# Performance work log

Hardware: AMD Instinct MI355X
Metric: run time of the kernel (lower is better)

The kernel has to match this reference:

```python
import jax, jax.numpy as jnp
import numpy as np

DIM = 1024
H = 16
HD = DIM // H  # 64
EPS = 1e-6
B, N = 1, 2048


def setup_inputs() -> dict:
    key = jax.random.key(0)
    k1, k2, k3 = jax.random.split(key, 3)
    x = jax.random.normal(k1, (B, N, DIM), dtype=jnp.float32)
    qkv_w = jax.random.normal(k2, (3 * DIM, DIM), dtype=jnp.float32) * 0.02
    proj_w = jax.random.normal(k3, (DIM, DIM), dtype=jnp.float32) * 0.02
    alpha_log = jnp.zeros((H,), dtype=jnp.float32)  # torch init: zeros
    beta_log = jnp.zeros((H,), dtype=jnp.float32)
    return {"x": x, "qkv_w": qkv_w, "proj_w": proj_w,
            "alpha_log": alpha_log, "beta_log": beta_log}


def reference(x, qkv_w, proj_w, alpha_log, beta_log):
    b, n, c = x.shape
    # fused qkv projection (nn.Linear: y = x @ W.T), split into per-head q,k,v
    qkv = (x @ qkv_w.T).reshape(b, n, 3, H, HD).transpose(2, 0, 3, 1, 4)
    q, k, v = qkv[0], qkv[1], qkv[2]  # each [b,h,n,d]
    # positive ReLU feature map
    phi_q = jax.nn.relu(q) + EPS
    phi_k = jax.nn.relu(k) + EPS
    # causal prefix-sum of outer products phi_k v^T -> running state S_n
    kv = jnp.einsum('bhnd,bhne->bhnde', phi_k, v)   # [b,h,n,d,d]
    S = jnp.cumsum(kv, axis=2)                       # prefix sums over n
    out = jnp.einsum('bhnd,bhnde->bhne', phi_q, S)   # [b,h,n,d]
    # SteLLA normalization: per-head alpha'*beta'*sqrt(d) * prefix length
    alpha_p = jax.nn.softplus(alpha_log) + 1e-6
    beta_p = jax.nn.softplus(beta_log) + 1e-6
    scale = (alpha_p * beta_p * jnp.sqrt(jnp.float32(HD))).reshape(1, H, 1, 1)
    pos = jnp.arange(1, n + 1, dtype=x.dtype).reshape(1, 1, n, 1)
    denom = jnp.maximum(scale * pos, EPS)
    out = out / denom
    out = out.transpose(0, 2, 1, 3).reshape(b, n, c)
    return out @ proj_w.T  # output projection (dropout=0 -> identity)
```

## Files before the change

kernel.cpp:

```cpp
#include <hip/hip_runtime.h>
#include <math.h>

#define DIM 1024
#define NH 16
#define HD 64
#define SEQ 2048
#define CHUNK 128
#define NCHUNK (SEQ / CHUNK)
#define QKV_COLS (3 * DIM)

typedef __attribute__((ext_vector_type(8))) short bf16x8;
typedef __attribute__((ext_vector_type(4))) float f32x4;

__device__ __forceinline__ unsigned short f2bf(float f) {
  unsigned int u = __float_as_uint(f);
  u += 0x7FFF + ((u >> 16) & 1);
  return (unsigned short)(u >> 16);
}
__device__ __forceinline__ float bf2f(unsigned short s) {
  return __uint_as_float(((unsigned int)s) << 16);
}
__device__ __forceinline__ int swzb(int byte, int row) {
  return byte ^ ((row & 7) << 4);
}

__global__ __launch_bounds__(256) void convert_all(const float* __restrict__ x,
                                                   const float* __restrict__ qw,
                                                   const float* __restrict__ pw,
                                                   unsigned short* __restrict__ xb,
                                                   unsigned short* __restrict__ qwb,
                                                   unsigned short* __restrict__ pwb) {
  const int b = blockIdx.x;
  const float* in; unsigned short* out; int i;
  if (b < 2048)      { in = x;  out = xb;  i = b * 256 + threadIdx.x; }
  else if (b < 5120) { in = qw; out = qwb; i = (b - 2048) * 256 + threadIdx.x; }
  else               { in = pw; out = pwb; i = (b - 5120) * 256 + threadIdx.x; }
  float4 v = reinterpret_cast<const float4*>(in)[i];
  ushort4 o;
  o.x = f2bf(v.x); o.y = f2bf(v.y); o.z = f2bf(v.z); o.w = f2bf(v.w);
  reinterpret_cast<ushort4*>(out)[i] = o;
}

template <int BM, int BN, typename OutT>
__global__ __launch_bounds__(256) void gemm3_bt(const unsigned short* __restrict__ A,
                                                const unsigned short* __restrict__ W,
                                                OutT* __restrict__ C,
                                                int M, int Nn, int K) {
  constexpr int BK = 32;
  constexpr int MFR = BM / 32;
  constexpr int NFR = BN / 32;
  constexpr int ACH = BM / 64;
  constexpr int BCH = BN / 64;
  __shared__ unsigned short As[3][BM * BK];
  __shared__ unsigned short Bs[3][BN * BK];
  const int tid  = threadIdx.x;
  const int lane = tid & 63;
  const int wv   = tid >> 6;
  const int row0 = blockIdx.y * BM;
  const int col0 = blockIdx.x * BN;
  const int ln15 = lane & 15;
  const int lhi  = lane >> 4;
  const int wr = (wv >> 1) * (BM / 2);
  const int wc = (wv & 1) * (BN / 2);

  f32x4 acc[MFR][NFR] = {};

  auto stage = [&](int buf, int t) {
    const int k0 = t * BK;
#pragma unroll
    for (int tt = 0; tt < ACH; ++tt) {
      const int chunk = wv * ACH + tt;
      const int lid = chunk * 64 + lane;
      const int r  = lid >> 2;
      const int ke = (lid & 3) << 3;
      __builtin_amdgcn_global_load_lds(
          (const __attribute__((address_space(1))) void*)&A[(size_t)(row0 + r) * K + k0 + ke],
          (__attribute__((address_space(3))) void*)&As[buf][chunk * 512], 16, 0, 0);
    }
#pragma unroll
    for (int tt = 0; tt < BCH; ++tt) {
      const int chunk = wv * BCH + tt;
      const int lid = chunk * 64 + lane;
      const int r  = lid >> 2;
      const int ke = (lid & 3) << 3;
      __builtin_amdgcn_global_load_lds(
          (const __attribute__((address_space(1))) void*)&W[(size_t)(col0 + r) * K + k0 + ke],
          (__attribute__((address_space(3))) void*)&Bs[buf][chunk * 512], 16, 0, 0);
    }
  };

  const int nt = K / BK;
  stage(0, 0);
  stage(1, 1);
  for (int t = 0; t < nt; ++t) {
    if (t < nt - 1) {
      constexpr int L = ACH + BCH;
      if constexpr (L == 4)      asm volatile("s_waitcnt vmcnt(4)" ::: "memory");
      else if constexpr (L == 3) asm volatile("s_waitcnt vmcnt(3)" ::: "memory");
      else                       asm volatile("s_waitcnt vmcnt(2)" ::: "memory");
    } else {
      asm volatile("s_waitcnt vmcnt(0)" ::: "memory");
    }
    __builtin_amdgcn_s_barrier();
    if (t + 2 < nt) stage((t + 2) % 3, t + 2);
    const int cur = t % 3;
    bf16x8 a[MFR], b[NFR];
#pragma unroll
    for (int m = 0; m < MFR; ++m)
      a[m] = *reinterpret_cast<const bf16x8*>(&As[cur][(wr + m * 16 + ln15) * BK + lhi * 8]);
#pragma unroll
    for (int n = 0; n < NFR; ++n)
      b[n] = *reinterpret_cast<const bf16x8*>(&Bs[cur][(wc + n * 16 + ln15) * BK + lhi * 8]);
#pragma unroll
    for (int m = 0; m < MFR; ++m)
#pragma unroll
      for (int n = 0; n < NFR; ++n)
        acc[m][n] = __builtin_amdgcn_mfma_f32_16x16x32_bf16(a[m], b[n], acc[m][n], 0, 0, 0);
  }

  const int crow = lhi * 4;
  const int ccol = ln15;
#pragma unroll
  for (int m = 0; m < MFR; ++m)
#pragma unroll
    for (int n = 0; n < NFR; ++n)
#pragma unroll
      for (int r = 0; r < 4; ++r) {
        const size_t idx = (size_t)(row0 + wr + m * 16 + crow + r) * Nn + col0 + wc + n * 16 + ccol;
        if constexpr (sizeof(OutT) == 2) C[idx] = (OutT)f2bf(acc[m][n][r]);
        else                             C[idx] = acc[m][n][r];
      }
}

__global__ __launch_bounds__(256) void ckv_mfma_kernel(const unsigned short* __restrict__ qkv,
                                                       float* __restrict__ ckv) {
  const int h = blockIdx.x / NCHUNK;
  const int c = blockIdx.x % NCHUNK;
  const int tid  = threadIdx.x;
  const int lane = tid & 63;
  const int w    = tid >> 6;
  const int ln15 = lane & 15;
  const int lhi  = lane >> 4;

  __shared__ unsigned short kst[HD * CHUNK];
  __shared__ unsigned short vt[HD * CHUNK];

  for (int i = tid; i < CHUNK * HD / 4; i += 256) {
    const int r = i >> 4;
    const int d4 = (i & 15) << 2;
    const size_t base = (size_t)(c * CHUNK + r) * QKV_COLS + h * HD + d4;
    ushort4 k4 = *reinterpret_cast<const ushort4*>(&qkv[base + DIM]);
    ushort4 v4 = *reinterpret_cast<const ushort4*>(&qkv[base + 2 * DIM]);
#pragma unroll
    for (int j = 0; j < 4; ++j) {
      const int d = d4 + j;
      *reinterpret_cast<unsigned short*>((char*)kst + swzb(d * 256 + r * 2, d)) =
          f2bf(fmaxf(bf2f((&k4.x)[j]), 0.f) + 1e-6f);
      *reinterpret_cast<unsigned short*>((char*)vt + swzb(d * 256 + r * 2, d)) = (&v4.x)[j];
    }
  }
  __syncthreads();

  f32x4 acc[4] = {};
#pragma unroll
  for (int ks = 0; ks < 4; ++ks) {
    const int dr = w * 16 + ln15;
    bf16x8 a = *reinterpret_cast<const bf16x8*>((char*)kst + swzb(dr * 256 + (ks * 32 + lhi * 8) * 2, dr));
#pragma unroll
    for (int et = 0; et < 4; ++et) {
      const int er = et * 16 + ln15;
      bf16x8 b = *reinterpret_cast<const bf16x8*>((char*)vt + swzb(er * 256 + (ks * 32 + lhi * 8) * 2, er));
      acc[et] = __builtin_amdgcn_mfma_f32_16x16x32_bf16(a, b, acc[et], 0, 0, 0);
    }
  }
  const size_t base = (size_t)(h * NCHUNK + c) * (HD * HD);
#pragma unroll
  for (int et = 0; et < 4; ++et)
#pragma unroll
    for (int r = 0; r < 4; ++r)
      ckv[base + (size_t)(w * 16 + lhi * 4 + r) * HD + et * 16 + ln15] = acc[et][r];
}

__global__ __launch_bounds__(256) void attn_mfma_kernel(const unsigned short* __restrict__ qkv,
                                                        const float* __restrict__ ckv,
                                                        const float* __restrict__ alpha_log,
                                                        const float* __restrict__ beta_log,
                                                        unsigned short* __restrict__ attn_out) {
  const int h = blockIdx.x / NCHUNK;
  const int c = blockIdx.x % NCHUNK;
  const int tid  = threadIdx.x;
  const int lane = tid & 63;
  const int w    = tid >> 6;
  const int ln15 = lane & 15;
  const int lhi  = lane >> 4;

  __shared__ unsigned short ks[CHUNK * HD];
  __shared__ unsigned short vst[HD * 256];
  __shared__ unsigned short ps[CHUNK * CHUNK];

  float sp[16];
#pragma unroll
  for (int p = 0; p < 16; ++p) sp[p] = 0.f;
  {
    const float* cb = ckv + (size_t)h * NCHUNK * (HD * HD) + tid * 16;
    for (int cc = 0; cc < c; ++cc) {
      const float4* p4 = reinterpret_cast<const float4*>(cb + (size_t)cc * (HD * HD));
#pragma unroll
      for (int q = 0; q < 4; ++q) {
        float4 t = p4[q];
        sp[q * 4 + 0] += t.x; sp[q * 4 + 1] += t.y;
        sp[q * 4 + 2] += t.z; sp[q * 4 + 3] += t.w;
      }
    }
  }
  {
    const int d = tid >> 2;
#pragma unroll
    for (int j = 0; j < 16; ++j) {
      const int e = (tid & 3) * 16 + j;
      const float sv = sp[j];
      const unsigned short hi = f2bf(sv);
      const unsigned short lo = f2bf(sv - bf2f(hi));
      *reinterpret_cast<unsigned short*>((char*)vst + swzb(e * 512 + d * 2, e)) = hi;
      *reinterpret_cast<unsigned short*>((char*)vst + swzb(e * 512 + (64 + d) * 2, e)) = lo;
    }
  }

  for (int i = tid; i < CHUNK * HD / 4; i += 256) {
    const int r = i >> 4;
    const int d4 = (i & 15) << 2;
    const size_t base = (size_t)(c * CHUNK + r) * QKV_COLS + h * HD + d4;
    ushort4 k4 = *reinterpret_cast<const ushort4*>(&qkv[base + DIM]);
    ushort4 v4 = *reinterpret_cast<const ushort4*>(&qkv[base + 2 * DIM]);
    ushort4 pk4;
    pk4.x = f2bf(fmaxf(bf2f(k4.x), 0.f) + 1e-6f);
    pk4.y = f2bf(fmaxf(bf2f(k4.y), 0.f) + 1e-6f);
    pk4.z = f2bf(fmaxf(bf2f(k4.z), 0.f) + 1e-6f);
    pk4.w = f2bf(fmaxf(bf2f(k4.w), 0.f) + 1e-6f);
    *reinterpret_cast<ushort4*>((char*)ks + swzb(r * 128 + d4 * 2, r)) = pk4;
#pragma unroll
    for (int j = 0; j < 4; ++j) {
      const int e = d4 + j;
      *reinterpret_cast<unsigned short*>((char*)vst + swzb(e * 512 + (128 + r) * 2, e)) = (&v4.x)[j];
    }
  }
  bf16x8 qf[2][2];
#pragma unroll
  for (int m = 0; m < 2; ++m)
#pragma unroll
    for (int kk = 0; kk < 2; ++kk) {
      const size_t gq = (size_t)(c * CHUNK + w * 32 + m * 16 + ln15) * QKV_COLS
                        + h * HD + kk * 32 + lhi * 8;
      bf16x8 raw = *reinterpret_cast<const bf16x8*>(&qkv[gq]);
#pragma unroll
      for (int j = 0; j < 8; ++j)
        raw[j] = (short)f2bf(fmaxf(bf2f((unsigned short)raw[j]), 0.f) + 1e-6f);
      qf[m][kk] = raw;
    }
  __syncthreads();

  f32x4 accs[2][8] = {};
#pragma unroll
  for (int j = 0; j < 8; ++j) {
    const int col = j * 16 + ln15;
    bf16x8 b0 = *reinterpret_cast<const bf16x8*>((char*)ks + swzb(col * 128 + lhi * 16, col));
    bf16x8 b1 = *reinterpret_cast<const bf16x8*>((char*)ks + swzb(col * 128 + 64 + lhi * 16, col));
#pragma unroll
    for (int m = 0; m < 2; ++m) {
      accs[m][j] = __builtin_amdgcn_mfma_f32_16x16x32_bf16(qf[m][0], b0, accs[m][j], 0, 0, 0);
      accs[m][j] = __builtin_amdgcn_mfma_f32_16x16x32_bf16(qf[m][1], b1, accs[m][j], 0, 0, 0);
    }
  }
#pragma unroll
  for (int m = 0; m < 2; ++m)
#pragma unroll
    for (int j = 0; j < 8; ++j)
#pragma unroll
      for (int r = 0; r < 4; ++r) {
        const int qrow = w * 32 + m * 16 + lhi * 4 + r;
        const int kcol = j * 16 + ln15;
        const float val = (qrow >= kcol) ? accs[m][j][r] : 0.f;
        *reinterpret_cast<unsigned short*>((char*)ps + swzb(qrow * 256 + kcol * 2, qrow)) = f2bf(val);
      }
  __syncthreads();

  f32x4 acco[2][4] = {};
#pragma unroll
  for (int kk = 0; kk < 8; ++kk) {
    bf16x8 a[2];
    if (kk < 4) {
#pragma unroll
      for (int m = 0; m < 2; ++m) a[m] = qf[m][kk & 1];
    } else {
#pragma unroll
      for (int m = 0; m < 2; ++m) {
        const int row = w * 32 + m * 16 + ln15;
        a[m] = *reinterpret_cast<const bf16x8*>((char*)ps + swzb(row * 256 + (kk - 4) * 64 + lhi * 16, row));
      }
    }
#pragma unroll
    for (int ct = 0; ct < 4; ++ct) {
      const int e = ct * 16 + ln15;
      bf16x8 b = *reinterpret_cast<const bf16x8*>((char*)vst + swzb(e * 512 + kk * 64 + lhi * 16, e));
#pragma unroll
      for (int m = 0; m < 2; ++m)
        acco[m][ct] = __builtin_amdgcn_mfma_f32_16x16x32_bf16(a[m], b, acco[m][ct], 0, 0, 0);
    }
  }

  const float ap = log1pf(expf(alpha_log[h])) + 1e-6f;
  const float bp = log1pf(expf(beta_log[h])) + 1e-6f;
  const float scale = ap * bp * 8.0f;
#pragma unroll
  for (int m = 0; m < 2; ++m)
#pragma unroll
    for (int ct = 0; ct < 4; ++ct)
#pragma unroll
      for (int r = 0; r < 4; ++r) {
        const int n = c * CHUNK + w * 32 + m * 16 + lhi * 4 + r;
        const float inv = 1.0f / fmaxf(scale * (float)(n + 1), 1e-6f);
        attn_out[(size_t)n * DIM + h * HD + ct * 16 + ln15] = f2bf(acco[m][ct][r] * inv);
      }
}

extern "C" void kernel_launch(void* const* d_in, const int* in_sizes, int n_in,
                              void* d_out, int out_size, void* d_ws, size_t ws_size,
                              hipStream_t stream) {
  const float* x        = (const float*)d_in[0];
  const float* qkv_w    = (const float*)d_in[1];
  const float* proj_w   = (const float*)d_in[2];
  const float* alpha_lg = (const float*)d_in[3];
  const float* beta_lg  = (const float*)d_in[4];
  float* out = (float*)d_out;

  char* ws = (char*)d_ws;
  size_t off = 0;
  unsigned short* qkvb = (unsigned short*)(ws + off); off += (size_t)SEQ * QKV_COLS * 2;
  float*          ckv  = (float*)         (ws + off); off += (size_t)NH * NCHUNK * HD * HD * 4;
  unsigned short* attn = (unsigned short*)(ws + off); off += (size_t)SEQ * DIM * 2;
  unsigned short* xb   = (unsigned short*)(ws + off); off += (size_t)SEQ * DIM * 2;
  unsigned short* qwb  = (unsigned short*)(ws + off); off += (size_t)QKV_COLS * DIM * 2;
  unsigned short* pwb  = (unsigned short*)(ws + off); off += (size_t)DIM * DIM * 2;

  convert_all<<<6144, 256, 0, stream>>>(x, qkv_w, proj_w, xb, qwb, pwb);
  gemm3_bt<64, 128, unsigned short><<<dim3(QKV_COLS / 128, SEQ / 64), 256, 0, stream>>>(
      xb, qwb, qkvb, SEQ, QKV_COLS, DIM);
  ckv_mfma_kernel<<<NH * NCHUNK, 256, 0, stream>>>(qkvb, ckv);
  attn_mfma_kernel<<<NH * NCHUNK, 256, 0, stream>>>(qkvb, ckv, alpha_lg, beta_lg, attn);
  gemm3_bt<128, 64, float><<<dim3(DIM / 64, SEQ / 128), 256, 0, stream>>>(
      attn, pwb, out, SEQ, DIM, DIM);
}
```

Baseline: 76.65 us.

## Fuse phi feature map into QKV GEMM epilogue and deepen GEMM pipelines

The ReLU+eps feature map for q and k now runs in the QKV GEMM epilogue, applied to columns below 2*DIM. The per-element conversions in the chunk-state and attention kernels are removed. The GEMM becomes templated on the number of LDS pipeline buffers, using 4 for the QKV GEMM and 6 for the output projection, with a matching vmcnt wait ladder. This is meant to hide more global-load latency and to remove redundant elementwise work. The cost is more LDS per block and possibly lower occupancy.

```diff
diff --git a/kernel.cpp b/kernel.cpp
--- a/kernel.cpp
+++ b/kernel.cpp
@@ -41,8 +41,8 @@
   reinterpret_cast<ushort4*>(out)[i] = o;
 }
 
-template <int BM, int BN, typename OutT>
-__global__ __launch_bounds__(256) void gemm3_bt(const unsigned short* __restrict__ A,
+template <int BM, int BN, int NBUF, bool PHI, typename OutT>
+__global__ __launch_bounds__(256) void gemmN_bt(const unsigned short* __restrict__ A,
                                                 const unsigned short* __restrict__ W,
                                                 OutT* __restrict__ C,
                                                 int M, int Nn, int K) {
@@ -51,8 +51,10 @@
   constexpr int NFR = BN / 32;
   constexpr int ACH = BM / 64;
   constexpr int BCH = BN / 64;
-  __shared__ unsigned short As[3][BM * BK];
-  __shared__ unsigned short Bs[3][BN * BK];
+  constexpr int L = ACH + BCH;
+  static_assert(L == 3, "vmcnt ladder assumes L==3");
+  __shared__ unsigned short As[NBUF][BM * BK];
+  __shared__ unsigned short Bs[NBUF][BN * BK];
   const int tid  = threadIdx.x;
   const int lane = tid & 63;
   const int wv   = tid >> 6;
@@ -90,20 +92,20 @@
   };
 
   const int nt = K / BK;
-  stage(0, 0);
-  stage(1, 1);
+#pragma unroll
+  for (int i = 0; i < NBUF - 1; ++i) stage(i, i);
   for (int t = 0; t < nt; ++t) {
-    if (t < nt - 1) {
-      constexpr int L = ACH + BCH;
-      if constexpr (L == 4)      asm volatile("s_waitcnt vmcnt(4)" ::: "memory");
-      else if constexpr (L == 3) asm volatile("s_waitcnt vmcnt(3)" ::: "memory");
-      else                       asm volatile("s_waitcnt vmcnt(2)" ::: "memory");
-    } else {
-      asm volatile("s_waitcnt vmcnt(0)" ::: "memory");
+    const int k = (nt - 1 - t) < (NBUF - 2) ? (nt - 1 - t) : (NBUF - 2);
+    switch (k) {
+      case 4:  asm volatile("s_waitcnt vmcnt(12)" ::: "memory"); break;
+      case 3:  asm volatile("s_waitcnt vmcnt(9)"  ::: "memory"); break;
+      case 2:  asm volatile("s_waitcnt vmcnt(6)"  ::: "memory"); break;
+      case 1:  asm volatile("s_waitcnt vmcnt(3)"  ::: "memory"); break;
+      default: asm volatile("s_waitcnt vmcnt(0)"  ::: "memory"); break;
     }
     __builtin_amdgcn_s_barrier();
-    if (t + 2 < nt) stage((t + 2) % 3, t + 2);
-    const int cur = t % 3;
+    if (t + NBUF - 1 < nt) stage((t + NBUF - 1) % NBUF, t + NBUF - 1);
+    const int cur = t % NBUF;
     bf16x8 a[MFR], b[NFR];
 #pragma unroll
     for (int m = 0; m < MFR; ++m)
@@ -126,9 +128,14 @@
     for (int n = 0; n < NFR; ++n)
 #pragma unroll
       for (int r = 0; r < 4; ++r) {
-        const size_t idx = (size_t)(row0 + wr + m * 16 + crow + r) * Nn + col0 + wc + n * 16 + ccol;
-        if constexpr (sizeof(OutT) == 2) C[idx] = (OutT)f2bf(acc[m][n][r]);
-        else                             C[idx] = acc[m][n][r];
+        const int gc = col0 + wc + n * 16 + ccol;
+        float v = acc[m][n][r];
+        if constexpr (PHI) {
+          if (gc < 2 * DIM) v = fmaxf(v, 0.f) + 1e-6f;
+        }
+        const size_t idx = (size_t)(row0 + wr + m * 16 + crow + r) * Nn + gc;
+        if constexpr (sizeof(OutT) == 2) C[idx] = (OutT)f2bf(v);
+        else                             C[idx] = v;
       }
 }
 
@@ -154,8 +161,7 @@
 #pragma unroll
     for (int j = 0; j < 4; ++j) {
       const int d = d4 + j;
-      *reinterpret_cast<unsigned short*>((char*)kst + swzb(d * 256 + r * 2, d)) =
-          f2bf(fmaxf(bf2f((&k4.x)[j]), 0.f) + 1e-6f);
+      *reinterpret_cast<unsigned short*>((char*)kst + swzb(d * 256 + r * 2, d)) = (&k4.x)[j];
       *reinterpret_cast<unsigned short*>((char*)vt + swzb(d * 256 + r * 2, d)) = (&v4.x)[j];
     }
   }
@@ -232,12 +238,7 @@
     const size_t base = (size_t)(c * CHUNK + r) * QKV_COLS + h * HD + d4;
     ushort4 k4 = *reinterpret_cast<const ushort4*>(&qkv[base + DIM]);
     ushort4 v4 = *reinterpret_cast<const ushort4*>(&qkv[base + 2 * DIM]);
-    ushort4 pk4;
-    pk4.x = f2bf(fmaxf(bf2f(k4.x), 0.f) + 1e-6f);
-    pk4.y = f2bf(fmaxf(bf2f(k4.y), 0.f) + 1e-6f);
-    pk4.z = f2bf(fmaxf(bf2f(k4.z), 0.f) + 1e-6f);
-    pk4.w = f2bf(fmaxf(bf2f(k4.w), 0.f) + 1e-6f);
-    *reinterpret_cast<ushort4*>((char*)ks + swzb(r * 128 + d4 * 2, r)) = pk4;
+    *reinterpret_cast<ushort4*>((char*)ks + swzb(r * 128 + d4 * 2, r)) = k4;
 #pragma unroll
     for (int j = 0; j < 4; ++j) {
       const int e = d4 + j;
@@ -251,11 +252,7 @@
     for (int kk = 0; kk < 2; ++kk) {
       const size_t gq = (size_t)(c * CHUNK + w * 32 + m * 16 + ln15) * QKV_COLS
                         + h * HD + kk * 32 + lhi * 8;
-      bf16x8 raw = *reinterpret_cast<const bf16x8*>(&qkv[gq]);
-#pragma unroll
-      for (int j = 0; j < 8; ++j)
-        raw[j] = (short)f2bf(fmaxf(bf2f((unsigned short)raw[j]), 0.f) + 1e-6f);
-      qf[m][kk] = raw;
+      qf[m][kk] = *reinterpret_cast<const bf16x8*>(&qkv[gq]);
     }
   __syncthreads();
 
@@ -343,10 +340,10 @@
   unsigned short* pwb  = (unsigned short*)(ws + off); off += (size_t)DIM * DIM * 2;
 
   convert_all<<<6144, 256, 0, stream>>>(x, qkv_w, proj_w, xb, qwb, pwb);
-  gemm3_bt<64, 128, unsigned short><<<dim3(QKV_COLS / 128, SEQ / 64), 256, 0, stream>>>(
+  gemmN_bt<64, 128, 4, true, unsigned short><<<dim3(QKV_COLS / 128, SEQ / 64), 256, 0, stream>>>(
       xb, qwb, qkvb, SEQ, QKV_COLS, DIM);
   ckv_mfma_kernel<<<NH * NCHUNK, 256, 0, stream>>>(qkvb, ckv);
   attn_mfma_kernel<<<NH * NCHUNK, 256, 0, stream>>>(qkvb, ckv, alpha_lg, beta_lg, attn);
-  gemm3_bt<128, 64, float><<<dim3(DIM / 64, SEQ / 128), 256, 0, stream>>>(
+  gemmN_bt<128, 64, 6, false, float><<<dim3(DIM / 64, SEQ / 128), 256, 0, stream>>>(
       attn, pwb, out, SEQ, DIM, DIM);
 }
```

Result: no change. 76.09 us (-0.7%).
